# Kernel optimization log

Hardware: AMD Instinct MI355X
Metric: run time of the kernel (lower is better)

Reference implementation:

```python
import jax, jax.numpy as jnp
import numpy as np

N_NODES = 50000
N_EDGES = 800000
IN_FEATS = 64
HIDDEN = 64
NUM_CLASSES = 64


def setup_inputs() -> dict:
    key = jax.random.key(0)
    ks = jax.random.split(key, 9)
    inputs = jax.random.normal(ks[0], (N_NODES, IN_FEATS), dtype=jnp.float32)
    W1 = jax.random.normal(ks[1], (HIDDEN, IN_FEATS), dtype=jnp.float32) * 0.05
    b1 = jax.random.normal(ks[2], (HIDDEN,), dtype=jnp.float32) * 0.05
    W2 = jax.random.normal(ks[3], (NUM_CLASSES, HIDDEN), dtype=jnp.float32) * 0.05
    b2 = jax.random.normal(ks[4], (NUM_CLASSES,), dtype=jnp.float32) * 0.05
    W3 = jax.random.normal(ks[5], (1, N_NODES), dtype=jnp.float32) * 0.01
    b3 = jax.random.normal(ks[6], (1,), dtype=jnp.float32) * 0.05
    src = jax.random.randint(ks[7], (N_EDGES,), 0, N_NODES, dtype=jnp.int32)
    dst = jax.random.randint(ks[8], (N_EDGES,), 0, N_NODES, dtype=jnp.int32)
    return {"inputs": inputs, "W1": W1, "b1": b1, "W2": W2, "b2": b2,
            "W3": W3, "b3": b3, "src": src, "dst": dst}


def _aggregate(h, src, dst):
    # DGL update_all with sum reduce: dst node gets sum of src features over in-edges
    msgs = h[src]  # [E, d] gather
    return jax.ops.segment_sum(msgs, dst, num_segments=N_NODES)


def reference(inputs, W1, b1, W2, b2, W3, b3, src, dst):
    # GNN layer 1: aggregate then linear
    h = _aggregate(inputs, src, dst) @ W1.T + b1  # [N, hidden]
    h = jax.nn.relu(h)
    # GNN layer 2
    h = _aggregate(h, src, dst) @ W2.T + b2       # [N, num_classes]
    # transpose -> [num_classes, N], linear over node dim -> [num_classes, 1]
    h = h.T @ W3.T + b3
    return jax.nn.sigmoid(h)
```

## Files before the change

kernel.cpp:

```cpp
#include <hip/hip_runtime.h>


#define FEATS 64
#define NW4   12500
#define NQ    12500
#define JD    128
#define JU    32
#define S_SLOT (64*16)

__device__ __forceinline__ unsigned f2bf(float x) {
    unsigned u = __float_as_uint(x);
    return (u + 0x7fffu + ((u >> 16) & 1u)) >> 16;
}
__device__ __forceinline__ float bf2f_lo(unsigned u) { return __uint_as_float(u << 16); }
__device__ __forceinline__ float bf2f_hi(unsigned u) { return __uint_as_float(u & 0xffff0000u); }

__global__ __launch_bounds__(256) void convert_bf16_kernel(
    const float* __restrict__ in, ushort* __restrict__ out, int n)
{
    int i = (blockIdx.x * 256 + threadIdx.x) * 4;
    if (i + 3 < n) {
        float4 v = *reinterpret_cast<const float4*>(&in[i]);
        ushort4 o;
        o.x = (ushort)f2bf(v.x); o.y = (ushort)f2bf(v.y);
        o.z = (ushort)f2bf(v.z); o.w = (ushort)f2bf(v.w);
        *reinterpret_cast<ushort4*>(&out[i]) = o;
    }
}

__global__ __launch_bounds__(512) void deg_hist_kernel(
    const int* __restrict__ dst, unsigned* __restrict__ cb8, int nEdges, int chunk)
{
    __shared__ unsigned cnt[NW4];
    int t = threadIdx.x, j = blockIdx.x;
    for (int l = t; l < NW4; l += 512) cnt[l] = 0u;
    __syncthreads();
    int beg = j * chunk, end = min(beg + chunk, nEdges);
    for (int e = beg + t; e < end; e += 512) {
        int d = dst[e];
        atomicAdd(&cnt[d >> 2], 1u << ((d & 3) * 8));
    }
    __syncthreads();
    unsigned* out = cb8 + (size_t)j * NW4;
    for (int l = t; l < NW4; l += 512) out[l] = cnt[l];
}

__global__ __launch_bounds__(512) void u_hist_kernel(
    const int* __restrict__ src, const int* __restrict__ dst,
    const float* __restrict__ W3, float* __restrict__ uJ, int nEdges, int chunk)
{
    __shared__ float ua[NQ];
    int t = threadIdx.x;
    int p = blockIdx.x & 3, j = blockIdx.x >> 2;
    for (int l = t; l < NQ; l += 512) ua[l] = 0.0f;
    __syncthreads();
    int beg = j * chunk, end = min(beg + chunk, nEdges);
    for (int e = beg + t; e < end; e += 512) {
        int s = src[e];
        if ((s & 3) == p) atomicAdd(&ua[s >> 2], W3[dst[e]]);
    }
    __syncthreads();
    float* out = uJ + (size_t)blockIdx.x * NQ;
    for (int l = t; l < NQ; l += 512) out[l] = ua[l];
}

__global__ __launch_bounds__(256) void bases_kernel(
    unsigned* __restrict__ cb8, const float* __restrict__ uJ,
    const float* __restrict__ W3, int* __restrict__ deg,
    float* __restrict__ u, float* __restrict__ partialPad)
{
    int w = blockIdx.x * 256 + threadIdx.x;
    float sv = 0.0f;
    if (w < NW4) {
        unsigned run = 0u;
        #pragma unroll 16
        for (int j = 0; j < JD; ++j) {
            unsigned c = cb8[(size_t)j * NW4 + w];
            cb8[(size_t)j * NW4 + w] = run;
            run += c;
        }
        int4 dg;
        dg.x = run & 0xff; dg.y = (run >> 8) & 0xff;
        dg.z = (run >> 16) & 0xff; dg.w = run >> 24;
        *reinterpret_cast<int4*>(&deg[w * 4]) = dg;

        float us0 = 0.f, us1 = 0.f, us2 = 0.f, us3 = 0.f;
        #pragma unroll 8
        for (int j = 0; j < JU; ++j) {
            us0 += uJ[(size_t)((j << 2) + 0) * NQ + w];
            us1 += uJ[(size_t)((j << 2) + 1) * NQ + w];
            us2 += uJ[(size_t)((j << 2) + 2) * NQ + w];
            us3 += uJ[(size_t)((j << 2) + 3) * NQ + w];
        }
        *reinterpret_cast<float4*>(&u[w * 4]) = make_float4(us0, us1, us2, us3);

        float4 w4 = *reinterpret_cast<const float4*>(&W3[w * 4]);
        sv = (w4.x + w4.y) + (w4.z + w4.w);
    }
    for (int o = 32; o > 0; o >>= 1) sv += __shfl_down(sv, o, 64);
    __shared__ float ws[4];
    if ((threadIdx.x & 63) == 0) ws[threadIdx.x >> 6] = sv;
    __syncthreads();
    if (threadIdx.x == 0)
        atomicAdd(&partialPad[S_SLOT], ws[0] + ws[1] + ws[2] + ws[3]);
}

__global__ __launch_bounds__(512) void edge_scatter_kernel(
    const int* __restrict__ src, const int* __restrict__ dst,
    const unsigned* __restrict__ cb8, ushort* __restrict__ srcSorted,
    int nEdges, int chunk)
{
    __shared__ unsigned cnt[NW4];
    int t = threadIdx.x, j = blockIdx.x;
    const unsigned* bb = cb8 + (size_t)j * NW4;
    for (int l = t; l < NW4; l += 512) cnt[l] = bb[l];
    __syncthreads();
    int beg = j * chunk, end = min(beg + chunk, nEdges);
    for (int e = beg + t; e < end; e += 512) {
        int d = dst[e], s = src[e];
        int sh = (d & 3) * 8;
        unsigned old = atomicAdd(&cnt[d >> 2], 1u << sh);
        int slot = (old >> sh) & 0xff;
        srcSorted[(d << 6) + slot] = (ushort)s;
    }
}

__global__ __launch_bounds__(256, 4) void fused_gather_linear_kernel(
    const ushort* __restrict__ featB, const ushort* __restrict__ srcSorted,
    const int* __restrict__ deg, const float* __restrict__ W1,
    const float* __restrict__ b1, const float* __restrict__ u,
    float* __restrict__ partialPad, int nNodes)
{
    __shared__ ushort idxbuf[4][8][64];
    __shared__ float rowbuf[4][8][FEATS];
    __shared__ float red[4][FEATS];
    int t = threadIdx.x, lane = t & 63, w = t >> 6;
    int g = lane >> 3;
    int l8 = lane & 7;

    float4 w1r[16];
    #pragma unroll
    for (int k4 = 0; k4 < 16; ++k4)
        w1r[k4] = *reinterpret_cast<const float4*>(&W1[lane * FEATS + k4 * 4]);
    float bias = b1[lane];

    int nOcts = (nNodes + 7) >> 3;
    int stride = gridDim.x * 4;
    float vacc = 0.0f;

    for (int oct = blockIdx.x * 4 + w; oct < nOcts; oct += stride) {
        int n_g = oct * 8 + g;
        int d = 0;
        float un = 0.0f;
        if (n_g < nNodes) {
            d = deg[n_g];
            un = u[n_g];
            uint4 ip = *reinterpret_cast<const uint4*>(&srcSorted[((size_t)n_g << 6) + l8 * 8]);
            *reinterpret_cast<uint4*>(&idxbuf[w][g][l8 * 8]) = ip;
        }
        __builtin_amdgcn_wave_barrier();

        int dm = d;
        dm = max(dm, __shfl_xor(dm, 8, 64));
        dm = max(dm, __shfl_xor(dm, 16, 64));
        dm = max(dm, __shfl_xor(dm, 32, 64));

        float a0=0.f,a1=0.f,a2=0.f,a3=0.f,a4=0.f,a5=0.f,a6=0.f,a7=0.f;
        for (int j = 0; j < dm; j += 4) {
            uint2 ids = *reinterpret_cast<const uint2*>(&idxbuf[w][g][j]);
            int i0 = ids.x & 0xffff, i1 = ids.x >> 16;
            int i2 = ids.y & 0xffff, i3 = ids.y >> 16;
            uint4 z = make_uint4(0u,0u,0u,0u);
            uint4 r0 = (j + 0 < d) ? *reinterpret_cast<const uint4*>(&featB[((size_t)i0 << 6) + l8 * 8]) : z;
            uint4 r1 = (j + 1 < d) ? *reinterpret_cast<const uint4*>(&featB[((size_t)i1 << 6) + l8 * 8]) : z;
            uint4 r2 = (j + 2 < d) ? *reinterpret_cast<const uint4*>(&featB[((size_t)i2 << 6) + l8 * 8]) : z;
            uint4 r3 = (j + 3 < d) ? *reinterpret_cast<const uint4*>(&featB[((size_t)i3 << 6) + l8 * 8]) : z;
            a0 += (bf2f_lo(r0.x) + bf2f_lo(r1.x)) + (bf2f_lo(r2.x) + bf2f_lo(r3.x));
            a1 += (bf2f_hi(r0.x) + bf2f_hi(r1.x)) + (bf2f_hi(r2.x) + bf2f_hi(r3.x));
            a2 += (bf2f_lo(r0.y) + bf2f_lo(r1.y)) + (bf2f_lo(r2.y) + bf2f_lo(r3.y));
            a3 += (bf2f_hi(r0.y) + bf2f_hi(r1.y)) + (bf2f_hi(r2.y) + bf2f_hi(r3.y));
            a4 += (bf2f_lo(r0.z) + bf2f_lo(r1.z)) + (bf2f_lo(r2.z) + bf2f_lo(r3.z));
            a5 += (bf2f_hi(r0.z) + bf2f_hi(r1.z)) + (bf2f_hi(r2.z) + bf2f_hi(r3.z));
            a6 += (bf2f_lo(r0.w) + bf2f_lo(r1.w)) + (bf2f_lo(r2.w) + bf2f_lo(r3.w));
            a7 += (bf2f_hi(r0.w) + bf2f_hi(r1.w)) + (bf2f_hi(r2.w) + bf2f_hi(r3.w));
        }
        *reinterpret_cast<float4*>(&rowbuf[w][g][l8 * 8])     = make_float4(a0,a1,a2,a3);
        *reinterpret_cast<float4*>(&rowbuf[w][g][l8 * 8 + 4]) = make_float4(a4,a5,a6,a7);
        __builtin_amdgcn_wave_barrier();

        #pragma unroll
        for (int gp = 0; gp < 8; ++gp) {
            float ug = __shfl(un, gp * 8, 64);
            float out = bias;
            #pragma unroll
            for (int k4 = 0; k4 < 16; ++k4) {
                float4 r = *reinterpret_cast<const float4*>(&rowbuf[w][gp][k4 * 4]);
                out += r.x * w1r[k4].x + r.y * w1r[k4].y
                     + r.z * w1r[k4].z + r.w * w1r[k4].w;
            }
            vacc += ug * fmaxf(out, 0.0f);
        }
        __builtin_amdgcn_wave_barrier();
    }

    red[w][lane] = vacc;
    __syncthreads();
    if (w == 0) {
        float vv = red[0][lane] + red[1][lane] + red[2][lane] + red[3][lane];
        atomicAdd(&partialPad[lane * 16], vv);
    }
}

__global__ __launch_bounds__(64) void finalize_kernel(
    const float* __restrict__ partialPad, const float* __restrict__ W2,
    const float* __restrict__ b2, const float* __restrict__ b3,
    float* __restrict__ out)
{
    __shared__ float v[FEATS];
    int c = threadIdx.x;
    v[c] = partialPad[c * 16];
    float s = partialPad[S_SLOT];
    __syncthreads();
    float acc = b3[0] + b2[c] * s;
    #pragma unroll
    for (int k = 0; k < FEATS; ++k)
        acc += W2[c * FEATS + k] * v[k];
    out[c] = 1.0f / (1.0f + expf(-acc));
}

extern "C" void kernel_launch(void* const* d_in, const int* in_sizes, int n_in,
                              void* d_out, int out_size, void* d_ws, size_t ws_size,
                              hipStream_t stream) {
    const float* inputs = (const float*)d_in[0];
    const float* W1     = (const float*)d_in[1];
    const float* b1     = (const float*)d_in[2];
    const float* W2     = (const float*)d_in[3];
    const float* b2     = (const float*)d_in[4];
    const float* W3     = (const float*)d_in[5];
    const float* b3     = (const float*)d_in[6];
    const int*   src    = (const int*)d_in[7];
    const int*   dst    = (const int*)d_in[8];

    int nNodes = in_sizes[0] / FEATS;
    int nEdges = in_sizes[7];

    unsigned* cb8       = (unsigned*)d_ws;
    float*    uJ        = (float*)(cb8 + (size_t)JD * NW4);
    int*      deg       = (int*)(uJ + (size_t)4 * JU * NQ);
    float*    u         = (float*)(deg + 4 * NW4);
    float*    partialPad= u + 4 * NW4;
    ushort*   featB     = (ushort*)(partialPad + 64 * 16 + 32);
    ushort*   srcSorted = featB + (size_t)4 * NW4 * FEATS;
    float*    outF      = (float*)d_out;

    int nFeat = nNodes * FEATS;
    int chD = (nEdges + JD - 1) / JD;
    int chU = (nEdges + JU - 1) / JU;

    hipMemsetAsync(partialPad, 0, (64 * 16 + 32) * sizeof(float), stream);

    convert_bf16_kernel<<<(nFeat / 4 + 255) / 256, 256, 0, stream>>>(inputs, featB, nFeat);
    deg_hist_kernel<<<JD, 512, 0, stream>>>(dst, cb8, nEdges, chD);
    u_hist_kernel<<<4 * JU, 512, 0, stream>>>(src, dst, W3, uJ, nEdges, chU);
    bases_kernel<<<(NW4 + 255) / 256, 256, 0, stream>>>(cb8, uJ, W3, deg, u, partialPad);
    edge_scatter_kernel<<<JD, 512, 0, stream>>>(src, dst, cb8, srcSorted, nEdges, chD);
    fused_gather_linear_kernel<<<1024, 256, 0, stream>>>(
        featB, srcSorted, deg, W1, b1, u, partialPad, nNodes);
    finalize_kernel<<<1, 64, 0, stream>>>(partialPad, W2, b2, b3, outF);
}
```

Baseline: 148.0 us.

## Software-pipeline neighbor gathers and launch one node-octet per wave

The gather loop in the fused aggregate+linear kernel is double-buffered. It issues the next group of four bf16 feature-row loads before accumulating the current group, so more memory requests are in flight. The persistent grid-stride loop is replaced by a grid sized to give each wave exactly one octet of nodes, and the min-blocks launch bound is dropped so the compiler can use more registers. Index rows are also only loaded for 8-entry chunks that fall within the node's degree. The extra live registers may lower occupancy, and the prefetch reads a few LDS index slots beyond the valid range, though the degree guards discard those values.

```diff
diff --git a/kernel.cpp b/kernel.cpp
--- a/kernel.cpp
+++ b/kernel.cpp
@@ -125,7 +125,7 @@
     }
 }
 
-__global__ __launch_bounds__(256, 4) void fused_gather_linear_kernel(
+__global__ __launch_bounds__(256) void fused_gather_linear_kernel(
     const ushort* __restrict__ featB, const ushort* __restrict__ srcSorted,
     const int* __restrict__ deg, const float* __restrict__ W1,
     const float* __restrict__ b1, const float* __restrict__ u,
@@ -145,18 +145,20 @@
     float bias = b1[lane];
 
     int nOcts = (nNodes + 7) >> 3;
-    int stride = gridDim.x * 4;
+    int oct = blockIdx.x * 4 + w;
     float vacc = 0.0f;
 
-    for (int oct = blockIdx.x * 4 + w; oct < nOcts; oct += stride) {
+    if (oct < nOcts) {
         int n_g = oct * 8 + g;
         int d = 0;
         float un = 0.0f;
         if (n_g < nNodes) {
             d = deg[n_g];
             un = u[n_g];
-            uint4 ip = *reinterpret_cast<const uint4*>(&srcSorted[((size_t)n_g << 6) + l8 * 8]);
-            *reinterpret_cast<uint4*>(&idxbuf[w][g][l8 * 8]) = ip;
+            if (l8 * 8 < d) {
+                uint4 ip = *reinterpret_cast<const uint4*>(&srcSorted[((size_t)n_g << 6) + l8 * 8]);
+                *reinterpret_cast<uint4*>(&idxbuf[w][g][l8 * 8]) = ip;
+            }
         }
         __builtin_amdgcn_wave_barrier();
 
@@ -166,24 +168,41 @@
         dm = max(dm, __shfl_xor(dm, 32, 64));
 
         float a0=0.f,a1=0.f,a2=0.f,a3=0.f,a4=0.f,a5=0.f,a6=0.f,a7=0.f;
-        for (int j = 0; j < dm; j += 4) {
-            uint2 ids = *reinterpret_cast<const uint2*>(&idxbuf[w][g][j]);
-            int i0 = ids.x & 0xffff, i1 = ids.x >> 16;
-            int i2 = ids.y & 0xffff, i3 = ids.y >> 16;
-            uint4 z = make_uint4(0u,0u,0u,0u);
-            uint4 r0 = (j + 0 < d) ? *reinterpret_cast<const uint4*>(&featB[((size_t)i0 << 6) + l8 * 8]) : z;
-            uint4 r1 = (j + 1 < d) ? *reinterpret_cast<const uint4*>(&featB[((size_t)i1 << 6) + l8 * 8]) : z;
-            uint4 r2 = (j + 2 < d) ? *reinterpret_cast<const uint4*>(&featB[((size_t)i2 << 6) + l8 * 8]) : z;
-            uint4 r3 = (j + 3 < d) ? *reinterpret_cast<const uint4*>(&featB[((size_t)i3 << 6) + l8 * 8]) : z;
-            a0 += (bf2f_lo(r0.x) + bf2f_lo(r1.x)) + (bf2f_lo(r2.x) + bf2f_lo(r3.x));
-            a1 += (bf2f_hi(r0.x) + bf2f_hi(r1.x)) + (bf2f_hi(r2.x) + bf2f_hi(r3.x));
-            a2 += (bf2f_lo(r0.y) + bf2f_lo(r1.y)) + (bf2f_lo(r2.y) + bf2f_lo(r3.y));
-            a3 += (bf2f_hi(r0.y) + bf2f_hi(r1.y)) + (bf2f_hi(r2.y) + bf2f_hi(r3.y));
-            a4 += (bf2f_lo(r0.z) + bf2f_lo(r1.z)) + (bf2f_lo(r2.z) + bf2f_lo(r3.z));
-            a5 += (bf2f_hi(r0.z) + bf2f_hi(r1.z)) + (bf2f_hi(r2.z) + bf2f_hi(r3.z));
-            a6 += (bf2f_lo(r0.w) + bf2f_lo(r1.w)) + (bf2f_lo(r2.w) + bf2f_lo(r3.w));
-            a7 += (bf2f_hi(r0.w) + bf2f_hi(r1.w)) + (bf2f_hi(r2.w) + bf2f_hi(r3.w));
-        }
+        uint4 r0,r1,r2,r3, s0,s1,s2,s3;
+        uint4 z = make_uint4(0u,0u,0u,0u);
+
+        #define LOADB(J, q0, q1, q2, q3)                                              \
+        {   int jj = (J);                                                             \
+            uint2 ids = *reinterpret_cast<const uint2*>(&idxbuf[w][g][jj]);           \
+            int i0 = ids.x & 0xffff, i1 = ids.x >> 16;                                \
+            int i2 = ids.y & 0xffff, i3 = ids.y >> 16;                                \
+            q0 = (jj + 0 < d) ? *reinterpret_cast<const uint4*>(&featB[((size_t)i0 << 6) + l8 * 8]) : z; \
+            q1 = (jj + 1 < d) ? *reinterpret_cast<const uint4*>(&featB[((size_t)i1 << 6) + l8 * 8]) : z; \
+            q2 = (jj + 2 < d) ? *reinterpret_cast<const uint4*>(&featB[((size_t)i2 << 6) + l8 * 8]) : z; \
+            q3 = (jj + 3 < d) ? *reinterpret_cast<const uint4*>(&featB[((size_t)i3 << 6) + l8 * 8]) : z; \
+        }
+        #define ACCB(q0, q1, q2, q3)                                                  \
+        {   a0 += (bf2f_lo(q0.x) + bf2f_lo(q1.x)) + (bf2f_lo(q2.x) + bf2f_lo(q3.x));  \
+            a1 += (bf2f_hi(q0.x) + bf2f_hi(q1.x)) + (bf2f_hi(q2.x) + bf2f_hi(q3.x));  \
+            a2 += (bf2f_lo(q0.y) + bf2f_lo(q1.y)) + (bf2f_lo(q2.y) + bf2f_lo(q3.y));  \
+            a3 += (bf2f_hi(q0.y) + bf2f_hi(q1.y)) + (bf2f_hi(q2.y) + bf2f_hi(q3.y));  \
+            a4 += (bf2f_lo(q0.z) + bf2f_lo(q1.z)) + (bf2f_lo(q2.z) + bf2f_lo(q3.z));  \
+            a5 += (bf2f_hi(q0.z) + bf2f_hi(q1.z)) + (bf2f_hi(q2.z) + bf2f_hi(q3.z));  \
+            a6 += (bf2f_lo(q0.w) + bf2f_lo(q1.w)) + (bf2f_lo(q2.w) + bf2f_lo(q3.w));  \
+            a7 += (bf2f_hi(q0.w) + bf2f_hi(q1.w)) + (bf2f_hi(q2.w) + bf2f_hi(q3.w));  \
+        }
+
+        LOADB(0, r0, r1, r2, r3);
+        LOADB(4, s0, s1, s2, s3);
+        for (int j = 0; j < dm; j += 8) {
+            ACCB(r0, r1, r2, r3);
+            LOADB(j + 8, r0, r1, r2, r3);
+            ACCB(s0, s1, s2, s3);
+            LOADB(j + 12, s0, s1, s2, s3);
+        }
+        #undef LOADB
+        #undef ACCB
+
         *reinterpret_cast<float4*>(&rowbuf[w][g][l8 * 8])     = make_float4(a0,a1,a2,a3);
         *reinterpret_cast<float4*>(&rowbuf[w][g][l8 * 8 + 4]) = make_float4(a4,a5,a6,a7);
         __builtin_amdgcn_wave_barrier();
@@ -200,7 +219,6 @@
             }
             vacc += ug * fmaxf(out, 0.0f);
         }
-        __builtin_amdgcn_wave_barrier();
     }
 
     red[w][lane] = vacc;
@@ -264,7 +282,8 @@
     u_hist_kernel<<<4 * JU, 512, 0, stream>>>(src, dst, W3, uJ, nEdges, chU);
     bases_kernel<<<(NW4 + 255) / 256, 256, 0, stream>>>(cb8, uJ, W3, deg, u, partialPad);
     edge_scatter_kernel<<<JD, 512, 0, stream>>>(src, dst, cb8, srcSorted, nEdges, chD);
-    fused_gather_linear_kernel<<<1024, 256, 0, stream>>>(
+    int nOcts = (nNodes + 7) >> 3;
+    fused_gather_linear_kernel<<<(nOcts + 3) / 4, 256, 0, stream>>>(
         featB, srcSorted, deg, W1, b1, u, partialPad, nNodes);
     finalize_kernel<<<1, 64, 0, stream>>>(partialPad, W2, b2, b3, outF);
 }
```

After: 149.2 us. No clear change (+0.8%).

## Merge histogram kernels, fold finalize into gather via ticket, one octet per wave

Applied to the files above, without the earlier changes.

The degree and u histograms now run as one launch. The u blocks split source nodes by parity instead of mod 4, so there are half as many blocks, each using a 25000-entry shared array. The separate finalize kernel is replaced by a last-block ticket inside the gather kernel, which removes one launch. The gather kernel's grid-stride loop is dropped in favor of one octet per wave over about 1563 blocks, and index loads are skipped for slots beyond the node's degree. Costs: a larger shared footprint per u block and more blocks that each reload W1 into registers.

```diff
diff --git a/kernel.cpp b/kernel.cpp
--- a/kernel.cpp
+++ b/kernel.cpp
@@ -3,7 +3,7 @@
 
 #define FEATS 64
 #define NW4   12500
-#define NQ    12500
+#define NHALF 25000
 #define JD    128
 #define JU    32
 #define S_SLOT (64*16)
@@ -28,40 +28,41 @@
     }
 }
 
-__global__ __launch_bounds__(512) void deg_hist_kernel(
-    const int* __restrict__ dst, unsigned* __restrict__ cb8, int nEdges, int chunk)
-{
-    __shared__ unsigned cnt[NW4];
-    int t = threadIdx.x, j = blockIdx.x;
-    for (int l = t; l < NW4; l += 512) cnt[l] = 0u;
-    __syncthreads();
-    int beg = j * chunk, end = min(beg + chunk, nEdges);
-    for (int e = beg + t; e < end; e += 512) {
-        int d = dst[e];
-        atomicAdd(&cnt[d >> 2], 1u << ((d & 3) * 8));
-    }
-    __syncthreads();
-    unsigned* out = cb8 + (size_t)j * NW4;
-    for (int l = t; l < NW4; l += 512) out[l] = cnt[l];
-}
-
-__global__ __launch_bounds__(512) void u_hist_kernel(
+__global__ __launch_bounds__(512) void hist_kernel(
     const int* __restrict__ src, const int* __restrict__ dst,
-    const float* __restrict__ W3, float* __restrict__ uJ, int nEdges, int chunk)
-{
-    __shared__ float ua[NQ];
+    const float* __restrict__ W3, unsigned* __restrict__ cb8,
+    float* __restrict__ uJ, int nEdges, int chD, int chU)
+{
+    __shared__ unsigned smem[NHALF];
     int t = threadIdx.x;
-    int p = blockIdx.x & 3, j = blockIdx.x >> 2;
-    for (int l = t; l < NQ; l += 512) ua[l] = 0.0f;
-    __syncthreads();
-    int beg = j * chunk, end = min(beg + chunk, nEdges);
-    for (int e = beg + t; e < end; e += 512) {
-        int s = src[e];
-        if ((s & 3) == p) atomicAdd(&ua[s >> 2], W3[dst[e]]);
-    }
-    __syncthreads();
-    float* out = uJ + (size_t)blockIdx.x * NQ;
-    for (int l = t; l < NQ; l += 512) out[l] = ua[l];
+    if (blockIdx.x < JD) {
+        unsigned* cnt = smem;
+        for (int l = t; l < NW4; l += 512) cnt[l] = 0u;
+        __syncthreads();
+        int j = blockIdx.x;
+        int beg = j * chD, end = min(beg + chD, nEdges);
+        for (int e = beg + t; e < end; e += 512) {
+            int d = dst[e];
+            atomicAdd(&cnt[d >> 2], 1u << ((d & 3) * 8));
+        }
+        __syncthreads();
+        unsigned* out = cb8 + (size_t)j * NW4;
+        for (int l = t; l < NW4; l += 512) out[l] = cnt[l];
+    } else {
+        float* ua = (float*)smem;
+        for (int l = t; l < NHALF; l += 512) ua[l] = 0.0f;
+        __syncthreads();
+        int b = blockIdx.x - JD;
+        int p = b & 1, j = b >> 1;
+        int beg = j * chU, end = min(beg + chU, nEdges);
+        for (int e = beg + t; e < end; e += 512) {
+            int s = src[e];
+            if ((s & 1) == p) atomicAdd(&ua[s >> 1], W3[dst[e]]);
+        }
+        __syncthreads();
+        float* out = uJ + (size_t)b * NHALF;
+        for (int l = t; l < NHALF; l += 512) out[l] = ua[l];
+    }
 }
 
 __global__ __launch_bounds__(256) void bases_kernel(
@@ -87,10 +88,12 @@
         float us0 = 0.f, us1 = 0.f, us2 = 0.f, us3 = 0.f;
         #pragma unroll 8
         for (int j = 0; j < JU; ++j) {
-            us0 += uJ[(size_t)((j << 2) + 0) * NQ + w];
-            us1 += uJ[(size_t)((j << 2) + 1) * NQ + w];
-            us2 += uJ[(size_t)((j << 2) + 2) * NQ + w];
-            us3 += uJ[(size_t)((j << 2) + 3) * NQ + w];
+            const float* a0 = uJ + (size_t)(2 * j)     * NHALF;
+            const float* a1 = uJ + (size_t)(2 * j + 1) * NHALF;
+            float2 e0 = *reinterpret_cast<const float2*>(&a0[2 * w]);
+            float2 e1 = *reinterpret_cast<const float2*>(&a1[2 * w]);
+            us0 += e0.x; us2 += e0.y;
+            us1 += e1.x; us3 += e1.y;
         }
         *reinterpret_cast<float4*>(&u[w * 4]) = make_float4(us0, us1, us2, us3);
 
@@ -129,11 +132,14 @@
     const ushort* __restrict__ featB, const ushort* __restrict__ srcSorted,
     const int* __restrict__ deg, const float* __restrict__ W1,
     const float* __restrict__ b1, const float* __restrict__ u,
-    float* __restrict__ partialPad, int nNodes)
+    float* __restrict__ partialPad, int* __restrict__ ticket,
+    const float* __restrict__ W2, const float* __restrict__ b2,
+    const float* __restrict__ b3, float* __restrict__ outF, int nNodes)
 {
     __shared__ ushort idxbuf[4][8][64];
     __shared__ float rowbuf[4][8][FEATS];
     __shared__ float red[4][FEATS];
+    __shared__ int lastFlag;
     int t = threadIdx.x, lane = t & 63, w = t >> 6;
     int g = lane >> 3;
     int l8 = lane & 7;
@@ -145,18 +151,20 @@
     float bias = b1[lane];
 
     int nOcts = (nNodes + 7) >> 3;
-    int stride = gridDim.x * 4;
+    int oct = blockIdx.x * 4 + w;
     float vacc = 0.0f;
 
-    for (int oct = blockIdx.x * 4 + w; oct < nOcts; oct += stride) {
+    if (oct < nOcts) {
         int n_g = oct * 8 + g;
         int d = 0;
         float un = 0.0f;
         if (n_g < nNodes) {
             d = deg[n_g];
             un = u[n_g];
-            uint4 ip = *reinterpret_cast<const uint4*>(&srcSorted[((size_t)n_g << 6) + l8 * 8]);
-            *reinterpret_cast<uint4*>(&idxbuf[w][g][l8 * 8]) = ip;
+            if (l8 * 8 < d) {
+                uint4 ip = *reinterpret_cast<const uint4*>(&srcSorted[((size_t)n_g << 6) + l8 * 8]);
+                *reinterpret_cast<uint4*>(&idxbuf[w][g][l8 * 8]) = ip;
+            }
         }
         __builtin_amdgcn_wave_barrier();
 
@@ -200,7 +208,6 @@
             }
             vacc += ug * fmaxf(out, 0.0f);
         }
-        __builtin_amdgcn_wave_barrier();
     }
 
     red[w][lane] = vacc;
@@ -209,23 +216,26 @@
         float vv = red[0][lane] + red[1][lane] + red[2][lane] + red[3][lane];
         atomicAdd(&partialPad[lane * 16], vv);
     }
-}
-
-__global__ __launch_bounds__(64) void finalize_kernel(
-    const float* __restrict__ partialPad, const float* __restrict__ W2,
-    const float* __restrict__ b2, const float* __restrict__ b3,
-    float* __restrict__ out)
-{
-    __shared__ float v[FEATS];
-    int c = threadIdx.x;
-    v[c] = partialPad[c * 16];
-    float s = partialPad[S_SLOT];
-    __syncthreads();
-    float acc = b3[0] + b2[c] * s;
-    #pragma unroll
-    for (int k = 0; k < FEATS; ++k)
-        acc += W2[c * FEATS + k] * v[k];
-    out[c] = 1.0f / (1.0f + expf(-acc));
+
+    if (t == 0) {
+        __threadfence();
+        int old = atomicAdd(ticket, 1);
+        lastFlag = (old == (int)gridDim.x - 1);
+    }
+    __syncthreads();
+    if (lastFlag && w == 0) {
+        float vk = __hip_atomic_load(&partialPad[lane * 16],
+                                     __ATOMIC_RELAXED, __HIP_MEMORY_SCOPE_AGENT);
+        float s  = __hip_atomic_load(&partialPad[S_SLOT],
+                                     __ATOMIC_RELAXED, __HIP_MEMORY_SCOPE_AGENT);
+        red[0][lane] = vk;
+        __builtin_amdgcn_wave_barrier();
+        float acc = b3[0] + b2[lane] * s;
+        #pragma unroll
+        for (int k = 0; k < FEATS; ++k)
+            acc += W2[lane * FEATS + k] * red[0][k];
+        outF[lane] = 1.0f / (1.0f + expf(-acc));
+    }
 }
 
 extern "C" void kernel_launch(void* const* d_in, const int* in_sizes, int n_in,
@@ -246,10 +256,11 @@
 
     unsigned* cb8       = (unsigned*)d_ws;
     float*    uJ        = (float*)(cb8 + (size_t)JD * NW4);
-    int*      deg       = (int*)(uJ + (size_t)4 * JU * NQ);
+    int*      deg       = (int*)(uJ + (size_t)2 * JU * NHALF);
     float*    u         = (float*)(deg + 4 * NW4);
     float*    partialPad= u + 4 * NW4;
-    ushort*   featB     = (ushort*)(partialPad + 64 * 16 + 32);
+    int*      ticket    = (int*)(partialPad + S_SLOT + 24);
+    ushort*   featB     = (ushort*)(partialPad + S_SLOT + 32);
     ushort*   srcSorted = featB + (size_t)4 * NW4 * FEATS;
     float*    outF      = (float*)d_out;
 
@@ -257,14 +268,14 @@
     int chD = (nEdges + JD - 1) / JD;
     int chU = (nEdges + JU - 1) / JU;
 
-    hipMemsetAsync(partialPad, 0, (64 * 16 + 32) * sizeof(float), stream);
+    hipMemsetAsync(partialPad, 0, (S_SLOT + 32) * sizeof(float), stream);
 
     convert_bf16_kernel<<<(nFeat / 4 + 255) / 256, 256, 0, stream>>>(inputs, featB, nFeat);
-    deg_hist_kernel<<<JD, 512, 0, stream>>>(dst, cb8, nEdges, chD);
-    u_hist_kernel<<<4 * JU, 512, 0, stream>>>(src, dst, W3, uJ, nEdges, chU);
+    hist_kernel<<<JD + 2 * JU, 512, 0, stream>>>(src, dst, W3, cb8, uJ, nEdges, chD, chU);
     bases_kernel<<<(NW4 + 255) / 256, 256, 0, stream>>>(cb8, uJ, W3, deg, u, partialPad);
     edge_scatter_kernel<<<JD, 512, 0, stream>>>(src, dst, cb8, srcSorted, nEdges, chD);
-    fused_gather_linear_kernel<<<1024, 256, 0, stream>>>(
-        featB, srcSorted, deg, W1, b1, u, partialPad, nNodes);
-    finalize_kernel<<<1, 64, 0, stream>>>(partialPad, W2, b2, b3, outF);
-}
+    int nOcts = (nNodes + 7) >> 3;
+    fused_gather_linear_kernel<<<(nOcts + 3) / 4, 256, 0, stream>>>(
+        featB, srcSorted, deg, W1, b1, u, partialPad, ticket,
+        W2, b2, b3, outF, nNodes);
+}
```

After: 161.7 us. 1.09x slower.
